# Kernel optimization log

Hardware: AMD Instinct MI355X
Metric: run time of the kernel (lower is better)

The kernel has to match this reference:

```python
import jax, jax.numpy as jnp
import numpy as np

EPS = 1e-8


def setup_inputs() -> dict:
    key = jax.random.key(0)
    k1, k2 = jax.random.split(key)
    a = jax.random.normal(k1, (1, 256, 128, 128), dtype=jnp.float32)
    b = jax.random.normal(k2, (1, 256, 128, 128), dtype=jnp.float32)
    return {"a": a, "b": b}


def reference(a, b):
    # a: [n, c, h, w] rendered feats; b: [n, c, h2, w2] style feats (n == 1)
    n, c, h, w = a.shape
    a_flat = a.reshape(n, c, -1)            # [n, c, hw]
    b_flat = b.reshape(n, c, -1)            # [n, c, h2w2]

    # argmin_cos_distance: channel-wise L2 normalize, cosine distance, argmin
    b_norm = jnp.sqrt((b_flat * b_flat).sum(1, keepdims=True) + EPS)
    b_n = b_flat / (b_norm + EPS)
    a_norm = jnp.sqrt((a_flat * a_flat).sum(1, keepdims=True) + EPS)
    a_n = a_flat / (a_norm + EPS)
    d_mat = 1.0 - jnp.einsum('ncp,ncq->npq', a_n, b_n)   # [n, hw, h2w2]
    z_best = jnp.argmin(d_mat, axis=2)                    # [n, hw]

    # nn_feat_replace: gather matched (unnormalized) style features
    idx = jnp.broadcast_to(z_best[:, None, :], b_flat.shape)
    target = jnp.take_along_axis(b_flat, idx, axis=2).reshape(n, c, h, w)

    # cos_loss(a, target): cosine distance over channel dim, mean over pixels
    an = jnp.sqrt((a * a).sum(1, keepdims=True))
    tn = jnp.sqrt((target * target).sum(1, keepdims=True))
    cossim = ((a / (an + EPS)) * (target / (tn + EPS))).sum(1)  # [n, h, w]
    return (1.0 - cossim).mean()
```

## Files before the change

kernel.cpp:

```cpp
#include <hip/hip_runtime.h>
#include <stdint.h>

#define EPS 1e-8f

constexpr int HW = 16384;
constexpr int BM = 128;
constexpr int NG = 2048;

typedef __attribute__((ext_vector_type(4))) float floatx4;
typedef __attribute__((ext_vector_type(8))) int   intx8;
typedef unsigned char u8;
typedef unsigned int u32;
typedef unsigned long long u64;

__device__ inline u32 pk4(float x0, float x1, float x2, float x3) {
    int t = __builtin_amdgcn_cvt_pk_fp8_f32(x0, x1, 0, false);
    t = __builtin_amdgcn_cvt_pk_fp8_f32(x2, x3, t, true);
    return (u32)t;
}

__device__ inline float getc(const float4& f, int j) {
    return (j == 0) ? f.x : (j == 1) ? f.y : (j == 2) ? f.z : f.w;
}

__global__ __launch_bounds__(256) void prep_kernel(const float* __restrict__ a,
                                                   const float* __restrict__ b,
                                                   float* __restrict__ sumsq_a,
                                                   float* __restrict__ sumsq_b,
                                                   u8* __restrict__ aF, u8* __restrict__ bF) {
    __shared__ float red[32][33];
    __shared__ float invb_sh[32];
    const int tid = threadIdx.x;
    const int pg = tid & 7, tc = tid >> 3;
    const int p0 = blockIdx.x * 32, pb = pg * 4;
    const int kb = tc >> 4, qg = (tc >> 2) & 3, e0 = (tc & 3) * 8;

    float4 bv[8];
    float ss0 = 0.f, ss1 = 0.f, ss2 = 0.f, ss3 = 0.f;
    #pragma unroll
    for (int i = 0; i < 8; ++i) {
        bv[i] = *(const float4*)&b[(size_t)(tc * 8 + i) * HW + p0 + pb];
        ss0 += bv[i].x * bv[i].x; ss1 += bv[i].y * bv[i].y;
        ss2 += bv[i].z * bv[i].z; ss3 += bv[i].w * bv[i].w;
    }
    red[tc][pb] = ss0; red[tc][pb + 1] = ss1; red[tc][pb + 2] = ss2; red[tc][pb + 3] = ss3;
    __syncthreads();
    if (tid < 32) {
        float B = 0.f;
        #pragma unroll
        for (int j = 0; j < 32; ++j) B += red[j][tid];
        sumsq_b[p0 + tid] = B;
        invb_sh[tid] = 1.0f / (sqrtf(B + EPS) + EPS);
    }
    __syncthreads();

    #pragma unroll
    for (int j = 0; j < 4; ++j) {
        const int p = p0 + pb + j;
        const int g = p >> 4, rp = p & 15;
        const float inv = invb_sh[pb + j];
        u64 wv = (u64)pk4(getc(bv[0], j) * inv, getc(bv[1], j) * inv,
                          getc(bv[2], j) * inv, getc(bv[3], j) * inv)
               | ((u64)pk4(getc(bv[4], j) * inv, getc(bv[5], j) * inv,
                           getc(bv[6], j) * inv, getc(bv[7], j) * inv) << 32);
        *(u64*)(bF + (((size_t)(g * 2 + kb)) << 11) + (qg * 16 + rp) * 32 + e0) = wv;
    }

    float4 av[8];
    ss0 = ss1 = ss2 = ss3 = 0.f;
    #pragma unroll
    for (int i = 0; i < 8; ++i) {
        av[i] = *(const float4*)&a[(size_t)(tc * 8 + i) * HW + p0 + pb];
        ss0 += av[i].x * av[i].x; ss1 += av[i].y * av[i].y;
        ss2 += av[i].z * av[i].z; ss3 += av[i].w * av[i].w;
    }
    #pragma unroll
    for (int j = 0; j < 4; ++j) {
        const int p = p0 + pb + j;
        const int g = p >> 4, rp = p & 15;
        u64 wv = (u64)pk4(getc(av[0], j), getc(av[1], j), getc(av[2], j), getc(av[3], j))
               | ((u64)pk4(getc(av[4], j), getc(av[5], j), getc(av[6], j), getc(av[7], j)) << 32);
        *(u64*)(aF + (((size_t)(g * 2 + kb)) << 11) + (qg * 16 + rp) * 32 + e0) = wv;
    }
    red[tc][pb] = ss0; red[tc][pb + 1] = ss1; red[tc][pb + 2] = ss2; red[tc][pb + 3] = ss3;
    __syncthreads();
    if (tid < 32) {
        float A = 0.f;
        #pragma unroll
        for (int j = 0; j < 32; ++j) A += red[j][tid];
        sumsq_a[p0 + tid] = A;
    }
}

__global__ __launch_bounds__(256, 3) void gemm_argmax(const u8* __restrict__ aF,
                                                      const u8* __restrict__ bF,
                                                      u64* __restrict__ packed) {
    const int tid = threadIdx.x;
    const int w = tid >> 6, lane = tid & 63;
    const int q4 = lane >> 4, r15 = lane & 15;
    const int wm = w >> 1, wn = w & 1;

    const u32 bid = blockIdx.x;
    const u32 ng = bid & 7;
    const u32 mt = bid >> 3;
    const int p0 = (int)mt * BM;

    const u8* gA = aF + (((size_t)(mt * 8 + wm * 4)) << 12) + (u32)lane * 32;
    intx8 Afr[4][2];
    #pragma unroll
    for (int mi = 0; mi < 4; ++mi)
        #pragma unroll
        for (int kb = 0; kb < 2; ++kb)
            Afr[mi][kb] = *(const intx8*)(gA + (u32)(mi * 2 + kb) * 2048u);

    const u8* gB = bF + (((size_t)(ng * 128 + wn * 2)) << 12) + (u32)lane * 32;

    float bestv[4][4];
    u32   bestq[4][4];
    #pragma unroll
    for (int mi = 0; mi < 4; ++mi)
        #pragma unroll
        for (int r = 0; r < 4; ++r) { bestv[mi][r] = -3.4e38f; bestq[mi][r] = 0; }

    u32 q0 = ng * 2048 + wn * 32 + (u32)r15;
    const floatx4 C64 = {64.f, 64.f, 64.f, 64.f};
    const int SCL = 0x7F7F7F7F;

    intx8 B0 = *(const intx8*)gB;
    intx8 B1;

    for (int qt = 0; qt < 32; ++qt) {
        const u8* gq = gB + (u32)qt * 16384u;
        floatx4 acc[4][2];

        B1 = *(const intx8*)(gq + 4096u);
        __builtin_amdgcn_s_setprio(1);
        #pragma unroll
        for (int mi = 0; mi < 4; ++mi)
            acc[mi][0] = __builtin_amdgcn_mfma_scale_f32_16x16x128_f8f6f4(
                Afr[mi][0], B0, C64, 0, 0, 0, SCL, 0, SCL);
        __builtin_amdgcn_s_setprio(0);

        B0 = *(const intx8*)(gq + 2048u);
        __builtin_amdgcn_s_setprio(1);
        #pragma unroll
        for (int mi = 0; mi < 4; ++mi)
            acc[mi][1] = __builtin_amdgcn_mfma_scale_f32_16x16x128_f8f6f4(
                Afr[mi][0], B1, C64, 0, 0, 0, SCL, 0, SCL);
        __builtin_amdgcn_s_setprio(0);

        B1 = *(const intx8*)(gq + 6144u);
        __builtin_amdgcn_s_setprio(1);
        #pragma unroll
        for (int mi = 0; mi < 4; ++mi)
            acc[mi][0] = __builtin_amdgcn_mfma_scale_f32_16x16x128_f8f6f4(
                Afr[mi][1], B0, acc[mi][0], 0, 0, 0, SCL, 0, SCL);
        __builtin_amdgcn_s_setprio(0);

        B0 = *(const intx8*)(gB + (u32)((qt + 1) & 31) * 16384u);
        __builtin_amdgcn_s_setprio(1);
        #pragma unroll
        for (int mi = 0; mi < 4; ++mi)
            acc[mi][1] = __builtin_amdgcn_mfma_scale_f32_16x16x128_f8f6f4(
                Afr[mi][1], B1, acc[mi][1], 0, 0, 0, SCL, 0, SCL);
        __builtin_amdgcn_s_setprio(0);

        #pragma unroll
        for (int mi = 0; mi < 4; ++mi)
            #pragma unroll
            for (int r = 0; r < 4; ++r) {
                float v = acc[mi][0][r];
                bool gt = v > bestv[mi][r];
                bestv[mi][r] = gt ? v : bestv[mi][r];
                bestq[mi][r] = gt ? q0 : bestq[mi][r];
            }
        #pragma unroll
        for (int mi = 0; mi < 4; ++mi)
            #pragma unroll
            for (int r = 0; r < 4; ++r) {
                float v = acc[mi][1][r];
                bool gt = v > bestv[mi][r];
                bestv[mi][r] = gt ? v : bestv[mi][r];
                bestq[mi][r] = gt ? (q0 + 16u) : bestq[mi][r];
            }
        q0 += 64u;
    }

    #pragma unroll
    for (int mi = 0; mi < 4; ++mi)
        #pragma unroll
        for (int r = 0; r < 4; ++r) {
            u64 pk = ((u64)__float_as_uint(bestv[mi][r]) << 32)
                   | (u64)(0xFFFFFFFFu - bestq[mi][r]);
            #pragma unroll
            for (int d = 1; d < 16; d <<= 1) {
                u64 o = __shfl_xor((unsigned long long)pk, d);
                pk = o > pk ? o : pk;
            }
            if (r15 == 0)
                atomicMax(&packed[p0 + wm * 64 + mi * 16 + q4 * 4 + r], pk);
        }
}

__global__ void loss_kernel(const u64* __restrict__ packed,
                            const float* __restrict__ sumsq_a, const float* __restrict__ sumsq_b,
                            float* __restrict__ out) {
    int p = blockIdx.x * 256 + threadIdx.x;
    u64 pk = packed[p];
    float s = __uint_as_float((u32)(pk >> 32)) - 64.0f;
    u32 q = 0xFFFFFFFFu - (u32)(pk & 0xFFFFFFFFull);
    float A = sumsq_a[p], B = sumsq_b[q];
    float dot = s * (sqrtf(B + EPS) + EPS);
    float cossim = dot / ((sqrtf(A) + EPS) * (sqrtf(B) + EPS));
    float v = (1.0f - cossim) * (1.0f / (float)HW);
    #pragma unroll
    for (int d = 1; d < 64; d <<= 1) v += __shfl_xor(v, d);
    if ((threadIdx.x & 63) == 0) atomicAdd(out, v);
}

extern "C" void kernel_launch(void* const* d_in, const int* in_sizes, int n_in,
                              void* d_out, int out_size, void* d_ws, size_t ws_size,
                              hipStream_t stream) {
    const float* a = (const float*)d_in[0];
    const float* b = (const float*)d_in[1];
    float* out = (float*)d_out;
    char* ws = (char*)d_ws;

    u8*    aF      = (u8*)ws;
    u8*    bF      = (u8*)(ws + (size_t)4 * 1024 * 1024);
    float* sumsq_a = (float*)(ws + (size_t)8 * 1024 * 1024);
    float* sumsq_b = sumsq_a + HW;
    u64*   packed  = (u64*)(sumsq_b + HW);

    hipMemsetAsync(out, 0, sizeof(float), stream);
    hipMemsetAsync(packed, 0, (size_t)HW * sizeof(u64), stream);

    prep_kernel<<<dim3(HW / 32), 256, 0, stream>>>(a, b, sumsq_a, sumsq_b, aF, bF);
    gemm_argmax<<<dim3((HW / BM) * (HW / NG)), 256, 0, stream>>>(aF, bF, packed);
    loss_kernel<<<dim3(HW / 256), 256, 0, stream>>>(packed, sumsq_a, sumsq_b, out);
}
```

Baseline: 156.6 us.

## Stage B tiles into LDS with async global_load_lds double buffering

The GEMM kernel stops loading B fragments per wave straight from global memory. It copies each 16KB B tile into a double-buffered LDS array with global_load_lds and syncs once per tile, so all four waves share one copy of the data. The fp8 packing layout changes to 16-byte chunks to fit that staging, and the prep kernel moves to 512 threads. The two memsets are folded into the prep kernel to remove extra launches. The cost is a block barrier every iteration and more LDS use, which may limit occupancy.

```diff
diff --git a/kernel.cpp b/kernel.cpp
--- a/kernel.cpp
+++ b/kernel.cpp
@@ -8,11 +8,18 @@
 constexpr int NG = 2048;
 
 typedef __attribute__((ext_vector_type(4))) float floatx4;
+typedef __attribute__((ext_vector_type(4))) int   intx4;
 typedef __attribute__((ext_vector_type(8))) int   intx8;
 typedef unsigned char u8;
 typedef unsigned int u32;
 typedef unsigned long long u64;
 
+typedef const __attribute__((address_space(1))) u32 gas_u32;
+typedef __attribute__((address_space(3))) u32 las_u32;
+__device__ inline void stage16(const void* g, void* l) {
+    __builtin_amdgcn_global_load_lds((gas_u32*)g, (las_u32*)l, 16, 0, 0);
+}
+
 __device__ inline u32 pk4(float x0, float x1, float x2, float x3) {
     int t = __builtin_amdgcn_cvt_pk_fp8_f32(x0, x1, 0, false);
     t = __builtin_amdgcn_cvt_pk_fp8_f32(x2, x3, t, true);
@@ -23,32 +30,45 @@
     return (j == 0) ? f.x : (j == 1) ? f.y : (j == 2) ? f.z : f.w;
 }
 
-__global__ __launch_bounds__(256) void prep_kernel(const float* __restrict__ a,
+__global__ __launch_bounds__(512) void prep_kernel(const float* __restrict__ a,
                                                    const float* __restrict__ b,
                                                    float* __restrict__ sumsq_a,
                                                    float* __restrict__ sumsq_b,
-                                                   u8* __restrict__ aF, u8* __restrict__ bF) {
-    __shared__ float red[32][33];
+                                                   u8* __restrict__ aF, u8* __restrict__ bF,
+                                                   u64* __restrict__ packed,
+                                                   float* __restrict__ out) {
+    __shared__ float red[64][33];
     __shared__ float invb_sh[32];
     const int tid = threadIdx.x;
     const int pg = tid & 7, tc = tid >> 3;
     const int p0 = blockIdx.x * 32, pb = pg * 4;
-    const int kb = tc >> 4, qg = (tc >> 2) & 3, e0 = (tc & 3) * 8;
-
-    float4 bv[8];
-    float ss0 = 0.f, ss1 = 0.f, ss2 = 0.f, ss3 = 0.f;
-    #pragma unroll
-    for (int i = 0; i < 8; ++i) {
-        bv[i] = *(const float4*)&b[(size_t)(tc * 8 + i) * HW + p0 + pb];
-        ss0 += bv[i].x * bv[i].x; ss1 += bv[i].y * bv[i].y;
-        ss2 += bv[i].z * bv[i].z; ss3 += bv[i].w * bv[i].w;
-    }
-    red[tc][pb] = ss0; red[tc][pb + 1] = ss1; red[tc][pb + 2] = ss2; red[tc][pb + 3] = ss3;
+    const int c0 = tc * 4;
+    const u32 fb = (u32)((c0 >> 7) * 2048 + ((c0 >> 4) & 1) * 1024 + (c0 & 15));
+    const u32 qr16 = (u32)(((c0 >> 5) & 3) * 16);
+
+    if (blockIdx.x < 32) packed[(size_t)blockIdx.x * 512 + tid] = 0ull;
+    if (blockIdx.x == 0 && tid == 0) *out = 0.f;
+
+    float4 bv[4], av[4];
+    #pragma unroll
+    for (int i = 0; i < 4; ++i)
+        bv[i] = *(const float4*)&b[(size_t)(c0 + i) * HW + p0 + pb];
+    #pragma unroll
+    for (int i = 0; i < 4; ++i)
+        av[i] = *(const float4*)&a[(size_t)(c0 + i) * HW + p0 + pb];
+
+    float s0 = 0.f, s1 = 0.f, s2 = 0.f, s3 = 0.f;
+    #pragma unroll
+    for (int i = 0; i < 4; ++i) {
+        s0 += bv[i].x * bv[i].x; s1 += bv[i].y * bv[i].y;
+        s2 += bv[i].z * bv[i].z; s3 += bv[i].w * bv[i].w;
+    }
+    red[tc][pb] = s0; red[tc][pb + 1] = s1; red[tc][pb + 2] = s2; red[tc][pb + 3] = s3;
     __syncthreads();
     if (tid < 32) {
         float B = 0.f;
         #pragma unroll
-        for (int j = 0; j < 32; ++j) B += red[j][tid];
+        for (int j = 0; j < 64; ++j) B += red[j][tid];
         sumsq_b[p0 + tid] = B;
         invb_sh[tid] = 1.0f / (sqrtf(B + EPS) + EPS);
     }
@@ -57,37 +77,30 @@
     #pragma unroll
     for (int j = 0; j < 4; ++j) {
         const int p = p0 + pb + j;
-        const int g = p >> 4, rp = p & 15;
         const float inv = invb_sh[pb + j];
-        u64 wv = (u64)pk4(getc(bv[0], j) * inv, getc(bv[1], j) * inv,
-                          getc(bv[2], j) * inv, getc(bv[3], j) * inv)
-               | ((u64)pk4(getc(bv[4], j) * inv, getc(bv[5], j) * inv,
-                           getc(bv[6], j) * inv, getc(bv[7], j) * inv) << 32);
-        *(u64*)(bF + (((size_t)(g * 2 + kb)) << 11) + (qg * 16 + rp) * 32 + e0) = wv;
-    }
-
-    float4 av[8];
-    ss0 = ss1 = ss2 = ss3 = 0.f;
-    #pragma unroll
-    for (int i = 0; i < 8; ++i) {
-        av[i] = *(const float4*)&a[(size_t)(tc * 8 + i) * HW + p0 + pb];
-        ss0 += av[i].x * av[i].x; ss1 += av[i].y * av[i].y;
-        ss2 += av[i].z * av[i].z; ss3 += av[i].w * av[i].w;
-    }
+        u32 wv = pk4(getc(bv[0], j) * inv, getc(bv[1], j) * inv,
+                     getc(bv[2], j) * inv, getc(bv[3], j) * inv);
+        *(u32*)(bF + ((size_t)(p >> 4) << 12) + fb + (qr16 + (u32)(p & 15)) * 16) = wv;
+    }
+
+    s0 = s1 = s2 = s3 = 0.f;
+    #pragma unroll
+    for (int i = 0; i < 4; ++i) {
+        s0 += av[i].x * av[i].x; s1 += av[i].y * av[i].y;
+        s2 += av[i].z * av[i].z; s3 += av[i].w * av[i].w;
+    }
+    red[tc][pb] = s0; red[tc][pb + 1] = s1; red[tc][pb + 2] = s2; red[tc][pb + 3] = s3;
     #pragma unroll
     for (int j = 0; j < 4; ++j) {
         const int p = p0 + pb + j;
-        const int g = p >> 4, rp = p & 15;
-        u64 wv = (u64)pk4(getc(av[0], j), getc(av[1], j), getc(av[2], j), getc(av[3], j))
-               | ((u64)pk4(getc(av[4], j), getc(av[5], j), getc(av[6], j), getc(av[7], j)) << 32);
-        *(u64*)(aF + (((size_t)(g * 2 + kb)) << 11) + (qg * 16 + rp) * 32 + e0) = wv;
-    }
-    red[tc][pb] = ss0; red[tc][pb + 1] = ss1; red[tc][pb + 2] = ss2; red[tc][pb + 3] = ss3;
+        u32 wv = pk4(getc(av[0], j), getc(av[1], j), getc(av[2], j), getc(av[3], j));
+        *(u32*)(aF + ((size_t)(p >> 4) << 12) + fb + (qr16 + (u32)(p & 15)) * 16) = wv;
+    }
     __syncthreads();
     if (tid < 32) {
         float A = 0.f;
         #pragma unroll
-        for (int j = 0; j < 32; ++j) A += red[j][tid];
+        for (int j = 0; j < 64; ++j) A += red[j][tid];
         sumsq_a[p0 + tid] = A;
     }
 }
@@ -95,6 +108,7 @@
 __global__ __launch_bounds__(256, 3) void gemm_argmax(const u8* __restrict__ aF,
                                                       const u8* __restrict__ bF,
                                                       u64* __restrict__ packed) {
+    __shared__ u8 sB[2][16384];
     const int tid = threadIdx.x;
     const int w = tid >> 6, lane = tid & 63;
     const int q4 = lane >> 4, r15 = lane & 15;
@@ -105,15 +119,23 @@
     const u32 mt = bid >> 3;
     const int p0 = (int)mt * BM;
 
-    const u8* gA = aF + (((size_t)(mt * 8 + wm * 4)) << 12) + (u32)lane * 32;
+    const u8* gA = aF + (((size_t)(mt * 8 + wm * 4)) << 12) + (u32)lane * 16;
     intx8 Afr[4][2];
     #pragma unroll
     for (int mi = 0; mi < 4; ++mi)
         #pragma unroll
-        for (int kb = 0; kb < 2; ++kb)
-            Afr[mi][kb] = *(const intx8*)(gA + (u32)(mi * 2 + kb) * 2048u);
-
-    const u8* gB = bF + (((size_t)(ng * 128 + wn * 2)) << 12) + (u32)lane * 32;
+        for (int kb = 0; kb < 2; ++kb) {
+            intx4 lo = *(const intx4*)(gA + (u32)(mi * 4096 + kb * 2048));
+            intx4 hi = *(const intx4*)(gA + (u32)(mi * 4096 + kb * 2048 + 1024));
+            Afr[mi][kb] = __builtin_shufflevector(lo, hi, 0, 1, 2, 3, 4, 5, 6, 7);
+        }
+
+    const u8* gQ = bF + ((size_t)ng << 19);
+    const u32 so = (u32)w * 4096u + (u32)lane * 16u;
+
+    #pragma unroll
+    for (int i = 0; i < 4; ++i)
+        stage16(gQ + so + (u32)(i * 1024), &sB[0][w * 4096 + i * 1024]);
 
     float bestv[4][4];
     u32   bestq[4][4];
@@ -126,39 +148,50 @@
     const floatx4 C64 = {64.f, 64.f, 64.f, 64.f};
     const int SCL = 0x7F7F7F7F;
 
-    intx8 B0 = *(const intx8*)gB;
-    intx8 B1;
-
+    __syncthreads();
+
+    int x = 0;
     for (int qt = 0; qt < 32; ++qt) {
-        const u8* gq = gB + (u32)qt * 16384u;
+        if (qt < 31) {
+            const u8* gs = gQ + (u32)(qt + 1) * 16384u + so;
+            u8* ls = &sB[x ^ 1][w * 4096];
+            #pragma unroll
+            for (int i = 0; i < 4; ++i)
+                stage16(gs + (u32)(i * 1024), ls + i * 1024);
+        }
+
+        const u8* Lb = &sB[x][(u32)(wn * 2) * 4096u + (u32)lane * 16u];
         floatx4 acc[4][2];
-
-        B1 = *(const intx8*)(gq + 4096u);
+        intx8 B0, B1;
+
+        { intx4 lo = *(const intx4*)(Lb);
+          intx4 hi = *(const intx4*)(Lb + 1024);
+          B0 = __builtin_shufflevector(lo, hi, 0, 1, 2, 3, 4, 5, 6, 7); }
+        { intx4 lo = *(const intx4*)(Lb + 4096);
+          intx4 hi = *(const intx4*)(Lb + 4096 + 1024);
+          B1 = __builtin_shufflevector(lo, hi, 0, 1, 2, 3, 4, 5, 6, 7); }
         __builtin_amdgcn_s_setprio(1);
         #pragma unroll
         for (int mi = 0; mi < 4; ++mi)
             acc[mi][0] = __builtin_amdgcn_mfma_scale_f32_16x16x128_f8f6f4(
                 Afr[mi][0], B0, C64, 0, 0, 0, SCL, 0, SCL);
-        __builtin_amdgcn_s_setprio(0);
-
-        B0 = *(const intx8*)(gq + 2048u);
-        __builtin_amdgcn_s_setprio(1);
         #pragma unroll
         for (int mi = 0; mi < 4; ++mi)
             acc[mi][1] = __builtin_amdgcn_mfma_scale_f32_16x16x128_f8f6f4(
                 Afr[mi][0], B1, C64, 0, 0, 0, SCL, 0, SCL);
         __builtin_amdgcn_s_setprio(0);
 
-        B1 = *(const intx8*)(gq + 6144u);
+        { intx4 lo = *(const intx4*)(Lb + 2048);
+          intx4 hi = *(const intx4*)(Lb + 2048 + 1024);
+          B0 = __builtin_shufflevector(lo, hi, 0, 1, 2, 3, 4, 5, 6, 7); }
+        { intx4 lo = *(const intx4*)(Lb + 4096 + 2048);
+          intx4 hi = *(const intx4*)(Lb + 4096 + 2048 + 1024);
+          B1 = __builtin_shufflevector(lo, hi, 0, 1, 2, 3, 4, 5, 6, 7); }
         __builtin_amdgcn_s_setprio(1);
         #pragma unroll
         for (int mi = 0; mi < 4; ++mi)
             acc[mi][0] = __builtin_amdgcn_mfma_scale_f32_16x16x128_f8f6f4(
                 Afr[mi][1], B0, acc[mi][0], 0, 0, 0, SCL, 0, SCL);
-        __builtin_amdgcn_s_setprio(0);
-
-        B0 = *(const intx8*)(gB + (u32)((qt + 1) & 31) * 16384u);
-        __builtin_amdgcn_s_setprio(1);
         #pragma unroll
         for (int mi = 0; mi < 4; ++mi)
             acc[mi][1] = __builtin_amdgcn_mfma_scale_f32_16x16x128_f8f6f4(
@@ -184,6 +217,9 @@
                 bestq[mi][r] = gt ? (q0 + 16u) : bestq[mi][r];
             }
         q0 += 64u;
+
+        __syncthreads();
+        x ^= 1;
     }
 
     #pragma unroll
@@ -232,10 +268,7 @@
     float* sumsq_b = sumsq_a + HW;
     u64*   packed  = (u64*)(sumsq_b + HW);
 
-    hipMemsetAsync(out, 0, sizeof(float), stream);
-    hipMemsetAsync(packed, 0, (size_t)HW * sizeof(u64), stream);
-
-    prep_kernel<<<dim3(HW / 32), 256, 0, stream>>>(a, b, sumsq_a, sumsq_b, aF, bF);
+    prep_kernel<<<dim3(HW / 32), 512, 0, stream>>>(a, b, sumsq_a, sumsq_b, aF, bF, packed, out);
     gemm_argmax<<<dim3((HW / BM) * (HW / NG)), 256, 0, stream>>>(aF, bF, packed);
     loss_kernel<<<dim3(HW / 256), 256, 0, stream>>>(packed, sumsq_a, sumsq_b, out);
 }
```

Measured after the change: 145.3 us. 1.08x faster.
